# Kernel optimization log

Hardware: AMD Instinct MI355X
Metric: run time of the kernel (lower is better)

Reference implementation:

```python
import jax, jax.numpy as jnp
import numpy as np

N_NODES = 100000
N_EDGES = 3200000
N_GRAPHS = 16
C = 64            # sage_channels
L = 6             # sage_layers
H = 32            # linear_channels
EPS = 1e-5

def layer_norm(x, g, b):
    mu = jnp.mean(x, axis=-1, keepdims=True)
    var = jnp.mean((x - mu) ** 2, axis=-1, keepdims=True)
    return (x - mu) * jax.lax.rsqrt(var + EPS) * g + b

def setup_inputs() -> dict:
    key = jax.random.key(0)
    ks = jax.random.split(key, 24)
    s = 1.0 / np.sqrt(C)
    inp = {
        'x': jax.random.normal(ks[0], (N_NODES, C), dtype=jnp.float32),
        'edge_index': jax.random.randint(ks[1], (2, N_EDGES), 0, N_NODES, dtype=jnp.int64),
        'batch': jnp.sort(jax.random.randint(ks[2], (N_NODES,), 0, N_GRAPHS, dtype=jnp.int64)),
        # 6 SAGE layers, each: lin_l (W+b) on aggregated, lin_r (W, no bias) on root, LayerNorm (g,b)
        'sage_Wl': jax.random.uniform(ks[3], (L, C, C), jnp.float32, -s, s),
        'sage_bl': jax.random.uniform(ks[4], (L, C), jnp.float32, -s, s),
        'sage_Wr': jax.random.uniform(ks[5], (L, C, C), jnp.float32, -s, s),
        'sage_g': jnp.ones((L, C), jnp.float32),
        'sage_b': jnp.zeros((L, C), jnp.float32),
        'mlp0_W': jax.random.uniform(ks[6], (C, H), jnp.float32, -s, s),
        'mlp0_b': jax.random.uniform(ks[7], (H,), jnp.float32, -s, s),
        'mlp0_g': jnp.ones((H,), jnp.float32),
        'mlp0_bn': jnp.zeros((H,), jnp.float32),
        'mlp_W': jax.random.uniform(ks[8], (3, H, H), jnp.float32, -1/np.sqrt(H), 1/np.sqrt(H)),
        'mlp_b': jax.random.uniform(ks[9], (3, H), jnp.float32, -1/np.sqrt(H), 1/np.sqrt(H)),
        'mlp_g': jnp.ones((3, H), jnp.float32),
        'mlp_bn': jnp.zeros((3, H), jnp.float32),
        'head_W': jax.random.uniform(ks[10], (H, 1), jnp.float32, -1/np.sqrt(H), 1/np.sqrt(H)),
        'head_b': jax.random.uniform(ks[11], (1,), jnp.float32, -1/np.sqrt(H), 1/np.sqrt(H)),
    }
    return inp

def reference(x, edge_index, batch, sage_Wl, sage_bl, sage_Wr, sage_g, sage_b,
              mlp0_W, mlp0_b, mlp0_g, mlp0_bn, mlp_W, mlp_b, mlp_g, mlp_bn, head_W, head_b):
    src, dst = edge_index[0], edge_index[1]
    # in-degree for mean aggregation (messages flow src -> dst), clamp to 1
    deg = jax.ops.segment_sum(jnp.ones((src.shape[0],), x.dtype), dst, num_segments=N_NODES)
    inv_deg = (1.0 / jnp.maximum(deg, 1.0))[:, None]
    h = x
    for i in range(L):
        msg_sum = jax.ops.segment_sum(h[src], dst, num_segments=N_NODES)  # [N, C]
        agg = msg_sum * inv_deg
        f = agg @ sage_Wl[i] + sage_bl[i] + h @ sage_Wr[i]
        f = jax.nn.gelu(f, approximate=False)
        f = layer_norm(f, sage_g[i], sage_b[i])
        h = f + h  # residual (all 6 appended blocks have with_residual=True)
    pooled = jax.ops.segment_max(h, batch, num_segments=N_GRAPHS)  # [G, C]
    z = layer_norm(jax.nn.gelu(pooled @ mlp0_W + mlp0_b, approximate=False), mlp0_g, mlp0_bn)
    for i in range(3):
        t = layer_norm(jax.nn.gelu(z @ mlp_W[i] + mlp_b[i], approximate=False), mlp_g[i], mlp_bn[i])
        z = t + z
    return z @ head_W + head_b  # [G, 1]
```

## Files before the change

### kernel.cpp

```cpp
#include <hip/hip_runtime.h>
#include <hip/hip_bf16.h>
#include <math.h>

#define N_NODES 100000
#define N_EDGES 3200000
#define N_GRAPHS 16
#define C 64
#define L 6
#define H 32
#define EPS 1e-5f
#define NPARTS 4
#define PART_DIV 25000
#define NBUCKETS (N_NODES * NPARTS)

static const int SCAN_BLOCKS = (NBUCKETS + 1023) / 1024;

__device__ __forceinline__ float gelu_exact(float x) {
    return 0.5f * x * (1.0f + erff(x * 0.70710678118654752440f));
}

__device__ __forceinline__ float wave_sum64(float v) {
#pragma unroll
    for (int m = 32; m >= 1; m >>= 1) v += __shfl_xor(v, m, 64);
    return v;
}

__device__ __forceinline__ float sum32(float v) {
#pragma unroll
    for (int m = 16; m >= 1; m >>= 1) v += __shfl_xor(v, m, 64);
    return v;
}

__device__ __forceinline__ unsigned short f32_to_bf16_rne(float f) {
    unsigned int u = __float_as_uint(f);
    u = (u + 0x7FFFu + ((u >> 16) & 1u)) >> 16;
    return (unsigned short)u;
}

#define ACC8(a0, a1, u)                                   \
    {                                                     \
        a0.x += __uint_as_float((u).x << 16);             \
        a0.y += __uint_as_float((u).x & 0xFFFF0000u);     \
        a0.z += __uint_as_float((u).y << 16);             \
        a0.w += __uint_as_float((u).y & 0xFFFF0000u);     \
        a1.x += __uint_as_float((u).z << 16);             \
        a1.y += __uint_as_float((u).z & 0xFFFF0000u);     \
        a1.z += __uint_as_float((u).w << 16);             \
        a1.w += __uint_as_float((u).w & 0xFFFF0000u);     \
    }


__global__ void k_count(const int* __restrict__ src, const int* __restrict__ dst,
                        int* __restrict__ degc, int* __restrict__ epos) {
    int i = blockIdx.x * blockDim.x + threadIdx.x;
    int stride = gridDim.x * blockDim.x;
    for (int e = i; e < N_EDGES; e += stride) {
        int part = src[e] / PART_DIV;
        int pos = __hip_atomic_fetch_add(&degc[dst[e] * NPARTS + part], 1,
                                         __ATOMIC_RELAXED, __HIP_MEMORY_SCOPE_AGENT);
        epos[e] = pos;
    }
}

__global__ __launch_bounds__(256) void k_scan1(const int* __restrict__ degc,
                                               int* __restrict__ scanned,
                                               int* __restrict__ bsum) {
    __shared__ int sc[2][256];
    int tid = threadIdx.x;
    int base = blockIdx.x * 1024 + tid * 4;
    int c0 = (base + 0 < NBUCKETS) ? degc[base + 0] : 0;
    int c1 = (base + 1 < NBUCKETS) ? degc[base + 1] : 0;
    int c2 = (base + 2 < NBUCKETS) ? degc[base + 2] : 0;
    int c3 = (base + 3 < NBUCKETS) ? degc[base + 3] : 0;
    int p0 = c0, p1 = p0 + c1, p2 = p1 + c2, p3 = p2 + c3;
    sc[0][tid] = p3;
    __syncthreads();
    int pb = 0;
    for (int offd = 1; offd < 256; offd <<= 1) {
        int v = sc[pb][tid];
        if (tid >= offd) v += sc[pb][tid - offd];
        sc[pb ^ 1][tid] = v;
        __syncthreads();
        pb ^= 1;
    }
    int incl = sc[pb][tid];
    int exth = incl - p3;
    if (base + 0 < NBUCKETS) scanned[base + 0] = exth + p0;
    if (base + 1 < NBUCKETS) scanned[base + 1] = exth + p1;
    if (base + 2 < NBUCKETS) scanned[base + 2] = exth + p2;
    if (base + 3 < NBUCKETS) scanned[base + 3] = exth + p3;
    if (tid == 255) bsum[blockIdx.x] = incl;
}

__global__ void k_scan2(const int* __restrict__ bsum, int* __restrict__ boff,
                        int* __restrict__ rowst) {
    int run = 0;
    for (int b = 0; b < SCAN_BLOCKS; ++b) { boff[b] = run; run += bsum[b]; }
    rowst[NBUCKETS] = run;
}

__global__ void k_scan3(const int* __restrict__ degc, const int* __restrict__ scanned,
                        const int* __restrict__ boff, int* __restrict__ rowst) {
    int i = blockIdx.x * blockDim.x + threadIdx.x;
    if (i < NBUCKETS) rowst[i] = boff[i >> 10] + scanned[i] - degc[i];
}

__global__ void k_fill(const int* __restrict__ src, const int* __restrict__ dst,
                       const int* __restrict__ rowst, const int* __restrict__ epos,
                       int* __restrict__ esrc) {
    int i = blockIdx.x * blockDim.x + threadIdx.x;
    int stride = gridDim.x * blockDim.x;
    for (int e = i; e < N_EDGES; e += stride) {
        int s = src[e];
        int part = s / PART_DIV;
        esrc[rowst[dst[e] * NPARTS + part] + epos[e]] = s;
    }
}

__global__ void k_cvt(const float* __restrict__ x, unsigned short* __restrict__ hbf) {
    int i = blockIdx.x * blockDim.x + threadIdx.x;
    int stride = gridDim.x * blockDim.x;
    for (int k = i; k < N_NODES * C / 4; k += stride) {
        float4 v = ((const float4*)x)[k];
        ushort4 o;
        o.x = f32_to_bf16_rne(v.x);
        o.y = f32_to_bf16_rne(v.y);
        o.z = f32_to_bf16_rne(v.z);
        o.w = f32_to_bf16_rne(v.w);
        ((ushort4*)hbf)[k] = o;
    }
}


__global__ __launch_bounds__(256) void k_agg(const unsigned short* __restrict__ hbf,
                                             const int* __restrict__ rowst,
                                             const int* __restrict__ esrc,
                                             float* __restrict__ agg) {
    const uint4* __restrict__ hb4 = (const uint4*)hbf;
    int wave = threadIdx.x >> 6, lane = threadIdx.x & 63;
    int n = blockIdx.x * 4 + wave;
    if (n >= N_NODES) return;
    int s0 = rowst[n * NPARTS], s1 = rowst[n * NPARTS + NPARTS];
    int esub = lane >> 3;
    int co = lane & 7;
    float4 accA0 = make_float4(0.f, 0.f, 0.f, 0.f), accA1 = accA0;
    float4 accB0 = accA0, accB1 = accA0;
    int j = s0;
    for (; j + 32 <= s1; j += 32) {
        int iA = esrc[j + 0 + esub];
        int iB = esrc[j + 8 + esub];
        int iC = esrc[j + 16 + esub];
        int iD = esrc[j + 24 + esub];
        uint4 a = hb4[(size_t)iA * 8 + co];
        uint4 b = hb4[(size_t)iB * 8 + co];
        uint4 c = hb4[(size_t)iC * 8 + co];
        uint4 d = hb4[(size_t)iD * 8 + co];
        ACC8(accA0, accA1, a);
        ACC8(accB0, accB1, b);
        ACC8(accA0, accA1, c);
        ACC8(accB0, accB1, d);
    }
    for (; j + 8 <= s1; j += 8) {
        int s = esrc[j + esub];
        uint4 a = hb4[(size_t)s * 8 + co];
        ACC8(accA0, accA1, a);
    }
    if (j < s1) {
        int jj = j + esub;
        bool v = jj < s1;
        int s = v ? esrc[jj] : 0;
        uint4 a = hb4[(size_t)s * 8 + co];
        if (!v) { a.x = 0; a.y = 0; a.z = 0; a.w = 0; }
        ACC8(accB0, accB1, a);
    }
    accA0.x += accB0.x; accA0.y += accB0.y; accA0.z += accB0.z; accA0.w += accB0.w;
    accA1.x += accB1.x; accA1.y += accB1.y; accA1.z += accB1.z; accA1.w += accB1.w;
#pragma unroll
    for (int m = 8; m <= 32; m <<= 1) {
        accA0.x += __shfl_xor(accA0.x, m, 64);
        accA0.y += __shfl_xor(accA0.y, m, 64);
        accA0.z += __shfl_xor(accA0.z, m, 64);
        accA0.w += __shfl_xor(accA0.w, m, 64);
        accA1.x += __shfl_xor(accA1.x, m, 64);
        accA1.y += __shfl_xor(accA1.y, m, 64);
        accA1.z += __shfl_xor(accA1.z, m, 64);
        accA1.w += __shfl_xor(accA1.w, m, 64);
    }
    int cnt = s1 - s0;
    float inv = 1.0f / (float)max(cnt, 1);
    if (lane < 8) {
        float4 r0 = make_float4(accA0.x * inv, accA0.y * inv, accA0.z * inv, accA0.w * inv);
        float4 r1 = make_float4(accA1.x * inv, accA1.y * inv, accA1.z * inv, accA1.w * inv);
        ((float4*)agg)[(size_t)n * 16 + co * 2 + 0] = r0;
        ((float4*)agg)[(size_t)n * 16 + co * 2 + 1] = r1;
    }
}


__global__ __launch_bounds__(256) void k_sage(const float* __restrict__ h,
                                              const float* __restrict__ agg,
                                              const float* __restrict__ Wl,
                                              const float* __restrict__ bl,
                                              const float* __restrict__ Wr,
                                              const float* __restrict__ gn,
                                              const float* __restrict__ bn,
                                              float* __restrict__ hout,
                                              unsigned short* __restrict__ hbf) {
    __shared__ float rowA[4][C];
    __shared__ float rowH[4][C];
    int lane = threadIdx.x & 63;
    int wave = threadIdx.x >> 6;
    float wl[C], wr[C];
#pragma unroll
    for (int j = 0; j < C; ++j) wl[j] = Wl[j * C + lane];
#pragma unroll
    for (int j = 0; j < C; ++j) wr[j] = Wr[j * C + lane];
    float blc = bl[lane], gc = gn[lane], bc = bn[lane];

    const float4* a4 = (const float4*)rowA[wave];
    const float4* h4s = (const float4*)rowH[wave];
    for (int n = blockIdx.x * 4 + wave; n < N_NODES; n += 2048 * 4) {
        float av = agg[(size_t)n * C + lane];
        float hv = h[(size_t)n * C + lane];
        rowA[wave][lane] = av;
        rowH[wave][lane] = hv;
        float acc = blc;
#pragma unroll
        for (int k4 = 0; k4 < C / 4; ++k4) {
            float4 a = a4[k4];
            float4 b = h4s[k4];
            acc += a.x * wl[4 * k4 + 0] + a.y * wl[4 * k4 + 1] +
                   a.z * wl[4 * k4 + 2] + a.w * wl[4 * k4 + 3];
            acc += b.x * wr[4 * k4 + 0] + b.y * wr[4 * k4 + 1] +
                   b.z * wr[4 * k4 + 2] + b.w * wr[4 * k4 + 3];
        }
        float f = gelu_exact(acc);
        float mu = wave_sum64(f) * (1.0f / C);
        float d = f - mu;
        float var = wave_sum64(d * d) * (1.0f / C);
        float y = d * rsqrtf(var + EPS) * gc + bc;
        float res = y + hv;
        hout[(size_t)n * C + lane] = res;
        hbf[(size_t)n * C + lane] = f32_to_bf16_rne(res);
    }
}


__global__ __launch_bounds__(256) void k_pool_partial(const float* __restrict__ h,
                                                      const int* __restrict__ batch,
                                                      float* __restrict__ partial) {
    __shared__ float pp[4][N_GRAPHS][C];
    int lane = threadIdx.x & 63, wave = threadIdx.x >> 6;
#pragma unroll
    for (int g = 0; g < N_GRAPHS; ++g) pp[wave][g][lane] = -INFINITY;
    int chunk = (N_NODES + gridDim.x - 1) / gridDim.x;
    int start = blockIdx.x * chunk;
    int end = min(start + chunk, N_NODES);
    for (int n = start + wave; n < end; n += 4) {
        int g = batch[n];
        float v = h[(size_t)n * C + lane];
        pp[wave][g][lane] = fmaxf(pp[wave][g][lane], v);
    }
    __syncthreads();
    for (int g = wave * 4; g < wave * 4 + 4; ++g) {
        float m = fmaxf(fmaxf(pp[0][g][lane], pp[1][g][lane]),
                        fmaxf(pp[2][g][lane], pp[3][g][lane]));
        partial[(size_t)blockIdx.x * (N_GRAPHS * C) + g * C + lane] = m;
    }
}

__global__ void k_pool_final(const float* __restrict__ partial, float* __restrict__ pooled) {
    int t = threadIdx.x;
    float m = -INFINITY;
    for (int b = 0; b < 128; ++b) m = fmaxf(m, partial[b * (N_GRAPHS * C) + t]);
    pooled[t] = m;
}


__global__ __launch_bounds__(512) void k_head(const float* __restrict__ pooled,
                                              const float* __restrict__ W0,
                                              const float* __restrict__ b0,
                                              const float* __restrict__ g0,
                                              const float* __restrict__ bn0,
                                              const float* __restrict__ W,
                                              const float* __restrict__ bb,
                                              const float* __restrict__ gg,
                                              const float* __restrict__ bnn,
                                              const float* __restrict__ hW,
                                              const float* __restrict__ hb,
                                              float* __restrict__ out) {
    __shared__ float ps[N_GRAPHS][C];
    __shared__ float zs[N_GRAPHS][H];
    int t = threadIdx.x;
    for (int i = t; i < N_GRAPHS * C; i += 512) ps[i >> 6][i & 63] = pooled[i];
    __syncthreads();
    int g = t >> 5, j = t & 31;
    float acc = b0[j];
#pragma unroll 8
    for (int k = 0; k < C; ++k) acc += ps[g][k] * W0[k * H + j];
    acc = gelu_exact(acc);
    float mu = sum32(acc) * (1.0f / H);
    float d = acc - mu;
    float var = sum32(d * d) * (1.0f / H);
    float z = d * rsqrtf(var + EPS) * g0[j] + bn0[j];
    zs[g][j] = z;
    __syncthreads();
    for (int i = 0; i < 3; ++i) {
        float a = bb[i * H + j];
#pragma unroll 8
        for (int k = 0; k < H; ++k) a += zs[g][k] * W[i * H * H + k * H + j];
        a = gelu_exact(a);
        float mu2 = sum32(a) * (1.0f / H);
        float d2 = a - mu2;
        float v2 = sum32(d2 * d2) * (1.0f / H);
        float tt = d2 * rsqrtf(v2 + EPS) * gg[i * H + j] + bnn[i * H + j];
        float zn = tt + zs[g][j];
        __syncthreads();
        zs[g][j] = zn;
        __syncthreads();
    }
    float hv = zs[g][j] * hW[j];
    hv = sum32(hv);
    if (j == 0) out[g] = hv + hb[0];
}


extern "C" void kernel_launch(void* const* d_in, const int* in_sizes, int n_in,
                              void* d_out, int out_size, void* d_ws, size_t ws_size,
                              hipStream_t stream) {
    const float* x    = (const float*)d_in[0];
    const int* edge   = (const int*)d_in[1];
    const int* batch  = (const int*)d_in[2];
    const float* sWl  = (const float*)d_in[3];
    const float* sbl  = (const float*)d_in[4];
    const float* sWr  = (const float*)d_in[5];
    const float* sg   = (const float*)d_in[6];
    const float* sb   = (const float*)d_in[7];
    const float* W0   = (const float*)d_in[8];
    const float* b0   = (const float*)d_in[9];
    const float* g0   = (const float*)d_in[10];
    const float* bn0  = (const float*)d_in[11];
    const float* mW   = (const float*)d_in[12];
    const float* mb   = (const float*)d_in[13];
    const float* mg   = (const float*)d_in[14];
    const float* mbn  = (const float*)d_in[15];
    const float* hW   = (const float*)d_in[16];
    const float* hb   = (const float*)d_in[17];
    float* out = (float*)d_out;

    const int* esrc_in = edge;
    const int* edst_in = edge + N_EDGES;

    char* ws = (char*)d_ws;
    size_t off = 0;
    auto alloc = [&](size_t bytes) {
        void* p = ws + off;
        off = (off + bytes + 1023) & ~(size_t)1023;
        return p;
    };
    float* h      = (float*)alloc((size_t)N_NODES * C * 4);
    float* agg    = (float*)alloc((size_t)N_NODES * C * 4);
    unsigned short* hbf = (unsigned short*)alloc((size_t)N_NODES * C * 2);
    int* degc     = (int*)alloc((size_t)NBUCKETS * 4);
    int* scanned  = (int*)alloc((size_t)NBUCKETS * 4);
    int* rowst    = (int*)alloc((size_t)(NBUCKETS + 1) * 4);
    int* esrc     = (int*)alloc((size_t)N_EDGES * 4);
    int* epos     = (int*)alloc((size_t)N_EDGES * 4);
    int* bsum     = (int*)alloc(512 * 4);
    int* boff     = (int*)alloc(512 * 4);
    float* part   = (float*)alloc((size_t)128 * N_GRAPHS * C * 4);
    float* pooled = (float*)alloc((size_t)N_GRAPHS * C * 4);
    (void)ws_size;

    hipMemsetAsync(degc, 0, (size_t)NBUCKETS * 4, stream);

    k_count<<<2048, 256, 0, stream>>>(esrc_in, edst_in, degc, epos);
    k_cvt<<<1600, 256, 0, stream>>>(x, hbf);
    k_scan1<<<SCAN_BLOCKS, 256, 0, stream>>>(degc, scanned, bsum);
    k_scan2<<<1, 1, 0, stream>>>(bsum, boff, rowst);
    k_scan3<<<(NBUCKETS + 255) / 256, 256, 0, stream>>>(degc, scanned, boff, rowst);
    k_fill<<<2048, 256, 0, stream>>>(esrc_in, edst_in, rowst, epos, esrc);

    for (int i = 0; i < L; ++i) {
        k_agg<<<N_NODES / 4, 256, 0, stream>>>(hbf, rowst, esrc, agg);
        k_sage<<<2048, 256, 0, stream>>>(i == 0 ? x : h, agg,
                                         sWl + (size_t)i * C * C, sbl + (size_t)i * C,
                                         sWr + (size_t)i * C * C, sg + (size_t)i * C,
                                         sb + (size_t)i * C, h, hbf);
    }

    k_pool_partial<<<128, 256, 0, stream>>>(h, batch, part);
    k_pool_final<<<1, 1024, 0, stream>>>(part, pooled);
    k_head<<<1, 512, 0, stream>>>(pooled, W0, b0, g0, bn0, mW, mb, mg, mbn, hW, hb, out);
}
```

Measured before the change: 1.199 ms.

## Split neighbor aggregation into four source-partition passes for cache locality

Neighbor aggregation now runs as four kernel launches per layer, each gathering only edges whose source falls in one quarter of the node range (the existing NPARTS buckets). Partial sums are accumulated in the fp32 agg buffer, and the last pass divides by the full degree. Each pass touches only about a quarter of the bf16 feature table (around 3.2 MB), so the random gathers should stay in L2. The cost is four times the launches and per-node bookkeeping, three extra read-modify-writes of agg per layer, and shorter per-bucket edge runs that leave the unrolled loop less work.

Measured after the change: 1.716 ms. +43.1%, slower.

```diff
diff --git a/kernel.cpp b/kernel.cpp
--- a/kernel.cpp
+++ b/kernel.cpp
@@ -132,33 +132,29 @@
 }
 
 
-__global__ __launch_bounds__(256) void k_agg(const unsigned short* __restrict__ hbf,
-                                             const int* __restrict__ rowst,
-                                             const int* __restrict__ esrc,
-                                             float* __restrict__ agg) {
+template <bool FIRST, bool LAST>
+__global__ __launch_bounds__(256) void k_aggp(const unsigned short* __restrict__ hbf,
+                                              const int* __restrict__ rowst,
+                                              const int* __restrict__ esrc,
+                                              float* __restrict__ agg,
+                                              int part) {
     const uint4* __restrict__ hb4 = (const uint4*)hbf;
     int wave = threadIdx.x >> 6, lane = threadIdx.x & 63;
     int n = blockIdx.x * 4 + wave;
     if (n >= N_NODES) return;
-    int s0 = rowst[n * NPARTS], s1 = rowst[n * NPARTS + NPARTS];
+    int s0 = rowst[n * NPARTS + part], s1 = rowst[n * NPARTS + part + 1];
     int esub = lane >> 3;
     int co = lane & 7;
     float4 accA0 = make_float4(0.f, 0.f, 0.f, 0.f), accA1 = accA0;
     float4 accB0 = accA0, accB1 = accA0;
     int j = s0;
-    for (; j + 32 <= s1; j += 32) {
+    for (; j + 16 <= s1; j += 16) {
         int iA = esrc[j + 0 + esub];
         int iB = esrc[j + 8 + esub];
-        int iC = esrc[j + 16 + esub];
-        int iD = esrc[j + 24 + esub];
         uint4 a = hb4[(size_t)iA * 8 + co];
         uint4 b = hb4[(size_t)iB * 8 + co];
-        uint4 c = hb4[(size_t)iC * 8 + co];
-        uint4 d = hb4[(size_t)iD * 8 + co];
         ACC8(accA0, accA1, a);
         ACC8(accB0, accB1, b);
-        ACC8(accA0, accA1, c);
-        ACC8(accB0, accB1, d);
     }
     for (; j + 8 <= s1; j += 8) {
         int s = esrc[j + esub];
@@ -186,13 +182,22 @@
         accA1.z += __shfl_xor(accA1.z, m, 64);
         accA1.w += __shfl_xor(accA1.w, m, 64);
     }
-    int cnt = s1 - s0;
-    float inv = 1.0f / (float)max(cnt, 1);
     if (lane < 8) {
-        float4 r0 = make_float4(accA0.x * inv, accA0.y * inv, accA0.z * inv, accA0.w * inv);
-        float4 r1 = make_float4(accA1.x * inv, accA1.y * inv, accA1.z * inv, accA1.w * inv);
-        ((float4*)agg)[(size_t)n * 16 + co * 2 + 0] = r0;
-        ((float4*)agg)[(size_t)n * 16 + co * 2 + 1] = r1;
+        float4* dst = ((float4*)agg) + (size_t)n * 16 + co * 2;
+        float4 r0 = accA0, r1 = accA1;
+        if (!FIRST) {
+            float4 p0 = dst[0], p1 = dst[1];
+            r0.x += p0.x; r0.y += p0.y; r0.z += p0.z; r0.w += p0.w;
+            r1.x += p1.x; r1.y += p1.y; r1.z += p1.z; r1.w += p1.w;
+        }
+        if (LAST) {
+            int cnt = rowst[n * NPARTS + NPARTS] - rowst[n * NPARTS];
+            float inv = 1.0f / (float)max(cnt, 1);
+            r0.x *= inv; r0.y *= inv; r0.z *= inv; r0.w *= inv;
+            r1.x *= inv; r1.y *= inv; r1.z *= inv; r1.w *= inv;
+        }
+        dst[0] = r0;
+        dst[1] = r1;
     }
 }
 
@@ -381,8 +386,12 @@
     k_scan3<<<(NBUCKETS + 255) / 256, 256, 0, stream>>>(degc, scanned, boff, rowst);
     k_fill<<<2048, 256, 0, stream>>>(esrc_in, edst_in, rowst, epos, esrc);
 
+    const int AGG_BLOCKS = N_NODES / 4;
     for (int i = 0; i < L; ++i) {
-        k_agg<<<N_NODES / 4, 256, 0, stream>>>(hbf, rowst, esrc, agg);
+        k_aggp<true, false><<<AGG_BLOCKS, 256, 0, stream>>>(hbf, rowst, esrc, agg, 0);
+        k_aggp<false, false><<<AGG_BLOCKS, 256, 0, stream>>>(hbf, rowst, esrc, agg, 1);
+        k_aggp<false, false><<<AGG_BLOCKS, 256, 0, stream>>>(hbf, rowst, esrc, agg, 2);
+        k_aggp<false, true><<<AGG_BLOCKS, 256, 0, stream>>>(hbf, rowst, esrc, agg, 3);
         k_sage<<<2048, 256, 0, stream>>>(i == 0 ? x : h, agg,
                                          sWl + (size_t)i * C * C, sbl + (size_t)i * C,
                                          sWr + (size_t)i * C * C, sg + (size_t)i * C,
```

## Fuse neighbor aggregation into SAGE layer kernel and drop source-partitioned CSR

Applied to the files above, without the earlier changes.

Merges the separate gather kernel (k_agg) into the per-layer SAGE kernel, so each wave gathers its node's neighbors, stages the mean in shared memory and does the matvec, GELU and LayerNorm directly. This removes the fp32 agg buffer write and re-read each layer. Two bf16 buffers now alternate between layers so the gather never reads rows being written. The CSR is simplified from 4 source-partitioned buckets per node to a single bucket per node, and the weights are held in registers as packed bf16 to cut register pressure. The cost is lost source locality in the gather, fewer waves in flight to hide gather latency, a smaller gather unroll, and extra rounding error from bf16 weights.

Measured after the change: 3.374 ms. +181.4%, slower.

```diff
diff --git a/kernel.cpp b/kernel.cpp
--- a/kernel.cpp
+++ b/kernel.cpp
@@ -9,11 +9,8 @@
 #define L 6
 #define H 32
 #define EPS 1e-5f
-#define NPARTS 4
-#define PART_DIV 25000
-#define NBUCKETS (N_NODES * NPARTS)
-
-static const int SCAN_BLOCKS = (NBUCKETS + 1023) / 1024;
+
+static const int SCAN_BLOCKS = (N_NODES + 1023) / 1024;
 
 __device__ __forceinline__ float gelu_exact(float x) {
     return 0.5f * x * (1.0f + erff(x * 0.70710678118654752440f));
@@ -50,14 +47,13 @@
     }
 
 
-__global__ void k_count(const int* __restrict__ src, const int* __restrict__ dst,
-                        int* __restrict__ degc, int* __restrict__ epos) {
+__global__ void k_count(const int* __restrict__ dst, int* __restrict__ degc,
+                        int* __restrict__ epos) {
     int i = blockIdx.x * blockDim.x + threadIdx.x;
     int stride = gridDim.x * blockDim.x;
     for (int e = i; e < N_EDGES; e += stride) {
-        int part = src[e] / PART_DIV;
-        int pos = __hip_atomic_fetch_add(&degc[dst[e] * NPARTS + part], 1,
-                                         __ATOMIC_RELAXED, __HIP_MEMORY_SCOPE_AGENT);
+        int pos = __hip_atomic_fetch_add(&degc[dst[e]], 1, __ATOMIC_RELAXED,
+                                         __HIP_MEMORY_SCOPE_AGENT);
         epos[e] = pos;
     }
 }
@@ -68,10 +64,10 @@
     __shared__ int sc[2][256];
     int tid = threadIdx.x;
     int base = blockIdx.x * 1024 + tid * 4;
-    int c0 = (base + 0 < NBUCKETS) ? degc[base + 0] : 0;
-    int c1 = (base + 1 < NBUCKETS) ? degc[base + 1] : 0;
-    int c2 = (base + 2 < NBUCKETS) ? degc[base + 2] : 0;
-    int c3 = (base + 3 < NBUCKETS) ? degc[base + 3] : 0;
+    int c0 = (base + 0 < N_NODES) ? degc[base + 0] : 0;
+    int c1 = (base + 1 < N_NODES) ? degc[base + 1] : 0;
+    int c2 = (base + 2 < N_NODES) ? degc[base + 2] : 0;
+    int c3 = (base + 3 < N_NODES) ? degc[base + 3] : 0;
     int p0 = c0, p1 = p0 + c1, p2 = p1 + c2, p3 = p2 + c3;
     sc[0][tid] = p3;
     __syncthreads();
@@ -85,10 +81,10 @@
     }
     int incl = sc[pb][tid];
     int exth = incl - p3;
-    if (base + 0 < NBUCKETS) scanned[base + 0] = exth + p0;
-    if (base + 1 < NBUCKETS) scanned[base + 1] = exth + p1;
-    if (base + 2 < NBUCKETS) scanned[base + 2] = exth + p2;
-    if (base + 3 < NBUCKETS) scanned[base + 3] = exth + p3;
+    if (base + 0 < N_NODES) scanned[base + 0] = exth + p0;
+    if (base + 1 < N_NODES) scanned[base + 1] = exth + p1;
+    if (base + 2 < N_NODES) scanned[base + 2] = exth + p2;
+    if (base + 3 < N_NODES) scanned[base + 3] = exth + p3;
     if (tid == 255) bsum[blockIdx.x] = incl;
 }
 
@@ -96,13 +92,13 @@
                         int* __restrict__ rowst) {
     int run = 0;
     for (int b = 0; b < SCAN_BLOCKS; ++b) { boff[b] = run; run += bsum[b]; }
-    rowst[NBUCKETS] = run;
+    rowst[N_NODES] = run;
 }
 
 __global__ void k_scan3(const int* __restrict__ degc, const int* __restrict__ scanned,
                         const int* __restrict__ boff, int* __restrict__ rowst) {
     int i = blockIdx.x * blockDim.x + threadIdx.x;
-    if (i < NBUCKETS) rowst[i] = boff[i >> 10] + scanned[i] - degc[i];
+    if (i < N_NODES) rowst[i] = boff[i >> 10] + scanned[i] - degc[i];
 }
 
 __global__ void k_fill(const int* __restrict__ src, const int* __restrict__ dst,
@@ -111,9 +107,7 @@
     int i = blockIdx.x * blockDim.x + threadIdx.x;
     int stride = gridDim.x * blockDim.x;
     for (int e = i; e < N_EDGES; e += stride) {
-        int s = src[e];
-        int part = s / PART_DIV;
-        esrc[rowst[dst[e] * NPARTS + part] + epos[e]] = s;
+        esrc[rowst[dst[e]] + epos[e]] = src[e];
     }
 }
 
@@ -132,107 +126,100 @@
 }
 
 
-__global__ __launch_bounds__(256) void k_agg(const unsigned short* __restrict__ hbf,
-                                             const int* __restrict__ rowst,
-                                             const int* __restrict__ esrc,
-                                             float* __restrict__ agg) {
-    const uint4* __restrict__ hb4 = (const uint4*)hbf;
-    int wave = threadIdx.x >> 6, lane = threadIdx.x & 63;
-    int n = blockIdx.x * 4 + wave;
-    if (n >= N_NODES) return;
-    int s0 = rowst[n * NPARTS], s1 = rowst[n * NPARTS + NPARTS];
+__global__ __launch_bounds__(256, 4) void k_sagg(
+        const float* __restrict__ hin,
+        const unsigned short* __restrict__ hbfR,
+        const int* __restrict__ rowst,
+        const int* __restrict__ esrc,
+        const float* __restrict__ Wl, const float* __restrict__ bl,
+        const float* __restrict__ Wr,
+        const float* __restrict__ gn, const float* __restrict__ bn,
+        float* __restrict__ hout,
+        unsigned short* __restrict__ hbfW) {
+    __shared__ float rowA[4][C];
+    __shared__ float rowH[4][C];
+    const uint4* __restrict__ hb4 = (const uint4*)hbfR;
+    int lane = threadIdx.x & 63;
+    int wave = threadIdx.x >> 6;
+
+    unsigned int wlp[C / 2], wrp[C / 2];
+#pragma unroll
+    for (int j = 0; j < C / 2; ++j) {
+        unsigned int lo = f32_to_bf16_rne(Wl[(2 * j) * C + lane]);
+        unsigned int hi = f32_to_bf16_rne(Wl[(2 * j + 1) * C + lane]);
+        wlp[j] = lo | (hi << 16);
+    }
+#pragma unroll
+    for (int j = 0; j < C / 2; ++j) {
+        unsigned int lo = f32_to_bf16_rne(Wr[(2 * j) * C + lane]);
+        unsigned int hi = f32_to_bf16_rne(Wr[(2 * j + 1) * C + lane]);
+        wrp[j] = lo | (hi << 16);
+    }
+    float blc = bl[lane], gc = gn[lane], bc = bn[lane];
+
     int esub = lane >> 3;
     int co = lane & 7;
-    float4 accA0 = make_float4(0.f, 0.f, 0.f, 0.f), accA1 = accA0;
-    float4 accB0 = accA0, accB1 = accA0;
-    int j = s0;
-    for (; j + 32 <= s1; j += 32) {
-        int iA = esrc[j + 0 + esub];
-        int iB = esrc[j + 8 + esub];
-        int iC = esrc[j + 16 + esub];
-        int iD = esrc[j + 24 + esub];
-        uint4 a = hb4[(size_t)iA * 8 + co];
-        uint4 b = hb4[(size_t)iB * 8 + co];
-        uint4 c = hb4[(size_t)iC * 8 + co];
-        uint4 d = hb4[(size_t)iD * 8 + co];
-        ACC8(accA0, accA1, a);
-        ACC8(accB0, accB1, b);
-        ACC8(accA0, accA1, c);
-        ACC8(accB0, accB1, d);
-    }
-    for (; j + 8 <= s1; j += 8) {
-        int s = esrc[j + esub];
-        uint4 a = hb4[(size_t)s * 8 + co];
-        ACC8(accA0, accA1, a);
-    }
-    if (j < s1) {
-        int jj = j + esub;
-        bool v = jj < s1;
-        int s = v ? esrc[jj] : 0;
-        uint4 a = hb4[(size_t)s * 8 + co];
-        if (!v) { a.x = 0; a.y = 0; a.z = 0; a.w = 0; }
-        ACC8(accB0, accB1, a);
-    }
-    accA0.x += accB0.x; accA0.y += accB0.y; accA0.z += accB0.z; accA0.w += accB0.w;
-    accA1.x += accB1.x; accA1.y += accB1.y; accA1.z += accB1.z; accA1.w += accB1.w;
-#pragma unroll
-    for (int m = 8; m <= 32; m <<= 1) {
-        accA0.x += __shfl_xor(accA0.x, m, 64);
-        accA0.y += __shfl_xor(accA0.y, m, 64);
-        accA0.z += __shfl_xor(accA0.z, m, 64);
-        accA0.w += __shfl_xor(accA0.w, m, 64);
-        accA1.x += __shfl_xor(accA1.x, m, 64);
-        accA1.y += __shfl_xor(accA1.y, m, 64);
-        accA1.z += __shfl_xor(accA1.z, m, 64);
-        accA1.w += __shfl_xor(accA1.w, m, 64);
-    }
-    int cnt = s1 - s0;
-    float inv = 1.0f / (float)max(cnt, 1);
-    if (lane < 8) {
-        float4 r0 = make_float4(accA0.x * inv, accA0.y * inv, accA0.z * inv, accA0.w * inv);
-        float4 r1 = make_float4(accA1.x * inv, accA1.y * inv, accA1.z * inv, accA1.w * inv);
-        ((float4*)agg)[(size_t)n * 16 + co * 2 + 0] = r0;
-        ((float4*)agg)[(size_t)n * 16 + co * 2 + 1] = r1;
-    }
-}
-
-
-__global__ __launch_bounds__(256) void k_sage(const float* __restrict__ h,
-                                              const float* __restrict__ agg,
-                                              const float* __restrict__ Wl,
-                                              const float* __restrict__ bl,
-                                              const float* __restrict__ Wr,
-                                              const float* __restrict__ gn,
-                                              const float* __restrict__ bn,
-                                              float* __restrict__ hout,
-                                              unsigned short* __restrict__ hbf) {
-    __shared__ float rowA[4][C];
-    __shared__ float rowH[4][C];
-    int lane = threadIdx.x & 63;
-    int wave = threadIdx.x >> 6;
-    float wl[C], wr[C];
-#pragma unroll
-    for (int j = 0; j < C; ++j) wl[j] = Wl[j * C + lane];
-#pragma unroll
-    for (int j = 0; j < C; ++j) wr[j] = Wr[j * C + lane];
-    float blc = bl[lane], gc = gn[lane], bc = bn[lane];
-
     const float4* a4 = (const float4*)rowA[wave];
     const float4* h4s = (const float4*)rowH[wave];
+
     for (int n = blockIdx.x * 4 + wave; n < N_NODES; n += 2048 * 4) {
-        float av = agg[(size_t)n * C + lane];
-        float hv = h[(size_t)n * C + lane];
-        rowA[wave][lane] = av;
+        int s0 = rowst[n], s1 = rowst[n + 1];
+        float4 accA0 = make_float4(0.f, 0.f, 0.f, 0.f), accA1 = accA0;
+        float4 accB0 = accA0, accB1 = accA0;
+        int j = s0;
+        for (; j + 16 <= s1; j += 16) {
+            int iA = esrc[j + 0 + esub];
+            int iB = esrc[j + 8 + esub];
+            uint4 a = hb4[(size_t)iA * 8 + co];
+            uint4 b = hb4[(size_t)iB * 8 + co];
+            ACC8(accA0, accA1, a);
+            ACC8(accB0, accB1, b);
+        }
+        for (; j + 8 <= s1; j += 8) {
+            int s = esrc[j + esub];
+            uint4 a = hb4[(size_t)s * 8 + co];
+            ACC8(accA0, accA1, a);
+        }
+        if (j < s1) {
+            int jj = j + esub;
+            bool v = jj < s1;
+            int s = v ? esrc[jj] : 0;
+            uint4 a = hb4[(size_t)s * 8 + co];
+            if (!v) { a.x = 0; a.y = 0; a.z = 0; a.w = 0; }
+            ACC8(accB0, accB1, a);
+        }
+        accA0.x += accB0.x; accA0.y += accB0.y; accA0.z += accB0.z; accA0.w += accB0.w;
+        accA1.x += accB1.x; accA1.y += accB1.y; accA1.z += accB1.z; accA1.w += accB1.w;
+#pragma unroll
+        for (int m = 8; m <= 32; m <<= 1) {
+            accA0.x += __shfl_xor(accA0.x, m, 64);
+            accA0.y += __shfl_xor(accA0.y, m, 64);
+            accA0.z += __shfl_xor(accA0.z, m, 64);
+            accA0.w += __shfl_xor(accA0.w, m, 64);
+            accA1.x += __shfl_xor(accA1.x, m, 64);
+            accA1.y += __shfl_xor(accA1.y, m, 64);
+            accA1.z += __shfl_xor(accA1.z, m, 64);
+            accA1.w += __shfl_xor(accA1.w, m, 64);
+        }
+        float hv = hin[(size_t)n * C + lane];
         rowH[wave][lane] = hv;
+        if (lane < 8) {
+            float inv = 1.0f / (float)max(s1 - s0, 1);
+            float4* dstA = ((float4*)rowA[wave]) + co * 2;
+            dstA[0] = make_float4(accA0.x * inv, accA0.y * inv, accA0.z * inv, accA0.w * inv);
+            dstA[1] = make_float4(accA1.x * inv, accA1.y * inv, accA1.z * inv, accA1.w * inv);
+        }
         float acc = blc;
 #pragma unroll
         for (int k4 = 0; k4 < C / 4; ++k4) {
             float4 a = a4[k4];
             float4 b = h4s[k4];
-            acc += a.x * wl[4 * k4 + 0] + a.y * wl[4 * k4 + 1] +
-                   a.z * wl[4 * k4 + 2] + a.w * wl[4 * k4 + 3];
-            acc += b.x * wr[4 * k4 + 0] + b.y * wr[4 * k4 + 1] +
-                   b.z * wr[4 * k4 + 2] + b.w * wr[4 * k4 + 3];
+            unsigned int l0 = wlp[2 * k4], l1 = wlp[2 * k4 + 1];
+            unsigned int r0 = wrp[2 * k4], r1 = wrp[2 * k4 + 1];
+            acc += a.x * __uint_as_float(l0 << 16) + a.y * __uint_as_float(l0 & 0xFFFF0000u);
+            acc += a.z * __uint_as_float(l1 << 16) + a.w * __uint_as_float(l1 & 0xFFFF0000u);
+            acc += b.x * __uint_as_float(r0 << 16) + b.y * __uint_as_float(r0 & 0xFFFF0000u);
+            acc += b.z * __uint_as_float(r1 << 16) + b.w * __uint_as_float(r1 & 0xFFFF0000u);
         }
         float f = gelu_exact(acc);
         float mu = wave_sum64(f) * (1.0f / C);
@@ -241,7 +228,7 @@
         float y = d * rsqrtf(var + EPS) * gc + bc;
         float res = y + hv;
         hout[(size_t)n * C + lane] = res;
-        hbf[(size_t)n * C + lane] = f32_to_bf16_rne(res);
+        hbfW[(size_t)n * C + lane] = f32_to_bf16_rne(res);
     }
 }
 
@@ -359,34 +346,36 @@
         return p;
     };
     float* h      = (float*)alloc((size_t)N_NODES * C * 4);
-    float* agg    = (float*)alloc((size_t)N_NODES * C * 4);
-    unsigned short* hbf = (unsigned short*)alloc((size_t)N_NODES * C * 2);
-    int* degc     = (int*)alloc((size_t)NBUCKETS * 4);
-    int* scanned  = (int*)alloc((size_t)NBUCKETS * 4);
-    int* rowst    = (int*)alloc((size_t)(NBUCKETS + 1) * 4);
+    unsigned short* hbf0 = (unsigned short*)alloc((size_t)N_NODES * C * 2);
+    unsigned short* hbf1 = (unsigned short*)alloc((size_t)N_NODES * C * 2);
+    int* degc     = (int*)alloc((size_t)N_NODES * 4);
+    int* scanned  = (int*)alloc((size_t)N_NODES * 4);
+    int* rowst    = (int*)alloc((size_t)(N_NODES + 1) * 4);
     int* esrc     = (int*)alloc((size_t)N_EDGES * 4);
     int* epos     = (int*)alloc((size_t)N_EDGES * 4);
-    int* bsum     = (int*)alloc(512 * 4);
-    int* boff     = (int*)alloc(512 * 4);
+    int* bsum     = (int*)alloc(128 * 4);
+    int* boff     = (int*)alloc(128 * 4);
     float* part   = (float*)alloc((size_t)128 * N_GRAPHS * C * 4);
     float* pooled = (float*)alloc((size_t)N_GRAPHS * C * 4);
     (void)ws_size;
 
-    hipMemsetAsync(degc, 0, (size_t)NBUCKETS * 4, stream);
-
-    k_count<<<2048, 256, 0, stream>>>(esrc_in, edst_in, degc, epos);
-    k_cvt<<<1600, 256, 0, stream>>>(x, hbf);
+    hipMemsetAsync(degc, 0, (size_t)N_NODES * 4, stream);
+
+    k_count<<<2048, 256, 0, stream>>>(edst_in, degc, epos);
+    k_cvt<<<1600, 256, 0, stream>>>(x, hbf0);
     k_scan1<<<SCAN_BLOCKS, 256, 0, stream>>>(degc, scanned, bsum);
     k_scan2<<<1, 1, 0, stream>>>(bsum, boff, rowst);
-    k_scan3<<<(NBUCKETS + 255) / 256, 256, 0, stream>>>(degc, scanned, boff, rowst);
+    k_scan3<<<(N_NODES + 255) / 256, 256, 0, stream>>>(degc, scanned, boff, rowst);
     k_fill<<<2048, 256, 0, stream>>>(esrc_in, edst_in, rowst, epos, esrc);
 
+    unsigned short* hbR = hbf0;
+    unsigned short* hbW = hbf1;
     for (int i = 0; i < L; ++i) {
-        k_agg<<<N_NODES / 4, 256, 0, stream>>>(hbf, rowst, esrc, agg);
-        k_sage<<<2048, 256, 0, stream>>>(i == 0 ? x : h, agg,
+        k_sagg<<<2048, 256, 0, stream>>>(i == 0 ? x : h, hbR, rowst, esrc,
                                          sWl + (size_t)i * C * C, sbl + (size_t)i * C,
                                          sWr + (size_t)i * C * C, sg + (size_t)i * C,
-                                         sb + (size_t)i * C, h, hbf);
+                                         sb + (size_t)i * C, h, hbW);
+        unsigned short* t = hbR; hbR = hbW; hbW = t;
     }
 
     k_pool_partial<<<128, 256, 0, stream>>>(h, batch, part);
```
